# Kernel tuning notes

Hardware: AMD Instinct MI355X
Metric: run time of the kernel (lower is better)

Reference implementation:

```python
import jax, jax.numpy as jnp
import numpy as np
import math

D_MODEL = 512
N_HEADS = 8
HEAD_DIM = D_MODEL // N_HEADS          # 64
RANK = max(N_HEADS, int(D_MODEL * 0.25))  # 128
RPH = RANK // N_HEADS                  # 16
LN_EPS = 1e-12


def _rope_tables(L, head_dim, dtype=jnp.float32):
    half = head_dim // 2
    theta = 1.0 / (10000.0 ** (jnp.arange(half, dtype=dtype) / half))
    ang = jnp.arange(L, dtype=dtype)[:, None] * theta[None, :]   # [L, half]
    return jnp.cos(ang), jnp.sin(ang)


def _apply_rope(x, cos, sin):
    # x: [B, L, H, D]; pairs (even, odd) along D form complex numbers
    B, L, H, D = x.shape
    xr = x.reshape(B, L, H, D // 2, 2)
    xre, xim = xr[..., 0], xr[..., 1]
    c = cos[None, :, None, :]
    s = sin[None, :, None, :]
    out_re = xre * c - xim * s
    out_im = xre * s + xim * c
    return jnp.stack([out_re, out_im], axis=-1).reshape(B, L, H, D)


def _tpa(x, mask, Wq, Wk, Wv, U, V):
    # x: [B, L, C]; mask: [B, L] bool; Wq/Wk/Wv: [rank, C]; U: [H, hd, rph]; V: [H, rph, hd]
    B, L, C = x.shape
    H, hd, rph = U.shape
    q_low = (x @ Wq.T).reshape(B, L, H, rph)
    k_low = (x @ Wk.T).reshape(B, L, H, rph)
    v_low = (x @ Wv.T).reshape(B, L, H, rph)
    q = jnp.einsum('hdr,blhr->blhd', U, q_low)
    k = jnp.einsum('hdr,blhr->blhd', U, k_low)
    cos, sin = _rope_tables(L, hd, x.dtype)
    q = _apply_rope(q, cos, sin)
    k = _apply_rope(k, cos, sin)
    attn = jnp.einsum('blhd,bmhd->bhlm', q, k) / math.sqrt(hd)
    attn = jnp.where(mask[:, None, None, :], attn, -jnp.inf)
    attn = jax.nn.softmax(attn, axis=-1)
    out = jnp.einsum('bhlm,bmhr->blhr', attn, v_low)
    out = jnp.einsum('blhr,hrd->blhd', out, V)
    return out.reshape(B, L, C)


def _layer_norm(x, g, b):
    m = jnp.mean(x, axis=-1, keepdims=True)
    v = jnp.mean(jnp.square(x - m), axis=-1, keepdims=True)
    return (x - m) / jnp.sqrt(v + LN_EPS) * g + b


def setup_inputs() -> dict:
    key = jax.random.key(0)
    ks = jax.random.split(key, 24)
    B, T, L, C = 4, 64, 256, D_MODEL

    def lin(k, shp, fan):
        return jax.random.normal(k, shp, jnp.float32) * (1.0 / math.sqrt(fan))

    inp = {
        'x': jax.random.normal(ks[0], (B, T, L, C), jnp.float32),
        'mask': jnp.ones((B, T, L), dtype=bool),
        'pe': jax.random.normal(ks[1], (L, C), jnp.float32),
        # time TPA params
        't_Wq': lin(ks[2], (RANK, C), C), 't_Wk': lin(ks[3], (RANK, C), C), 't_Wv': lin(ks[4], (RANK, C), C),
        't_U': lin(ks[5], (N_HEADS, HEAD_DIM, RPH), HEAD_DIM + RPH),
        't_V': lin(ks[6], (N_HEADS, RPH, HEAD_DIM), HEAD_DIM + RPH),
        # aa TPA params
        'a_Wq': lin(ks[7], (RANK, C), C), 'a_Wk': lin(ks[8], (RANK, C), C), 'a_Wv': lin(ks[9], (RANK, C), C),
        'a_U': lin(ks[10], (N_HEADS, HEAD_DIM, RPH), HEAD_DIM + RPH),
        'a_V': lin(ks[11], (N_HEADS, RPH, HEAD_DIM), HEAD_DIM + RPH),
        # layer norms
        'ln1_g': jnp.ones((C,)), 'ln1_b': jnp.zeros((C,)),
        'ln2_g': jnp.ones((C,)), 'ln2_b': jnp.zeros((C,)),
        'ln3_g': jnp.ones((C,)), 'ln3_b': jnp.zeros((C,)),
        # proj + gates
        'proj_W': lin(ks[12], (C, C), C), 'proj_b': jnp.zeros((C,)),
        'gt_W': lin(ks[13], (C, 2 * C), 2 * C), 'gt_b': jnp.zeros((C,)),
        'ga_W': lin(ks[14], (C, 2 * C), 2 * C), 'ga_b': jnp.zeros((C,)),
    }
    return inp


def reference(x, mask, pe,
              t_Wq, t_Wk, t_Wv, t_U, t_V,
              a_Wq, a_Wk, a_Wv, a_U, a_V,
              ln1_g, ln1_b, ln2_g, ln2_b, ln3_g, ln3_b,
              proj_W, proj_b, gt_W, gt_b, ga_W, ga_b):
    B, T, L, C = x.shape
    residual_time = x
    xn = _layer_norm(x, ln1_g, ln1_b)
    # temporal attention over T, batched over (B*L)
    x_time = jnp.transpose(xn, (0, 2, 1, 3)).reshape(B * L, T, C)
    m_time = jnp.transpose(mask, (0, 2, 1)).reshape(B * L, T)
    x_time = _tpa(x_time, m_time, t_Wq, t_Wk, t_Wv, t_U, t_V)
    x_time = jnp.transpose(x_time.reshape(B, L, T, C), (0, 2, 1, 3))
    gate = jax.nn.sigmoid(jnp.concatenate([residual_time, x_time], axis=-1) @ gt_W.T + gt_b)
    x_time = gate * residual_time + (1.0 - gate) * x_time

    residual_aa = x_time
    xn2 = _layer_norm(x_time, ln2_g, ln2_b)
    # spatial (amino-acid) attention over L, batched over (B*T)
    x_aa = xn2.reshape(B * T, L, C)
    m_aa = mask.reshape(B * T, L)
    x_aa = _tpa(x_aa, m_aa, a_Wq, a_Wk, a_Wv, a_U, a_V)
    x_aa = x_aa.reshape(B, T, L, C)
    gate = jax.nn.sigmoid(jnp.concatenate([residual_aa, x_aa], axis=-1) @ ga_W.T + ga_b)
    x_aa = gate * residual_aa + (1.0 - gate) * x_aa

    residual_proj = x_aa
    x_aa = _layer_norm(x_aa, ln3_g, ln3_b) @ proj_W.T + proj_b  # dropout is identity in eval
    return x_aa + residual_proj
```

## Files before the change

kernel.cpp:

```cpp
#include <hip/hip_runtime.h>

typedef __attribute__((ext_vector_type(8))) short short8;
typedef __attribute__((ext_vector_type(4))) short short4v;
typedef __attribute__((ext_vector_type(4))) float f32x4;
typedef unsigned short ushort_t;
typedef unsigned int uint_t;

#define B_ 4
#define T_ 64
#define L_ 256
#define C_ 512
#define H_ 8
#define NTOK 65536

__device__ __forceinline__ ushort_t f2bf(float f) {
    uint_t u = __float_as_uint(f);
    u += 0x7FFFu + ((u >> 16) & 1u);
    return (ushort_t)(u >> 16);
}
__device__ __forceinline__ float bf2f(ushort_t u) {
    return __uint_as_float((uint_t)u << 16);
}
__device__ __forceinline__ uint_t pk2(float a, float b) {
    return (uint_t)f2bf(a) | ((uint_t)f2bf(b) << 16);
}
__device__ __forceinline__ void gload16(const ushort_t* __restrict__ g, ushort_t* l) {
    __builtin_amdgcn_global_load_lds(
        (const __attribute__((address_space(1))) void*)g,
        (__attribute__((address_space(3))) void*)l,
        16, 0, 0);
}

__global__ void rope_tables(float* __restrict__ cosT, float* __restrict__ sinT) {
    int idx = blockIdx.x * 256 + threadIdx.x;
    if (idx >= 256 * 32) return;
    int pos = idx >> 5, i = idx & 31;
    float theta = powf(10000.f, -(float)i * (1.f / 32.f));
    float ang = (float)pos * theta;
    float sv, cv;
    sincosf(ang, &sv, &cv);
    cosT[idx] = cv;
    sinT[idx] = sv;
}

__global__ void packw(const float* __restrict__ src, ushort_t* __restrict__ dst, int n) {
    const int i = (blockIdx.x * 256 + threadIdx.x) * 4;
    if (i < n) {
        float4 v = *(const float4*)(src + i);
        *(uint2*)(dst + i) = make_uint2(pk2(v.x, v.y), pk2(v.z, v.w));
    }
}

template<bool RAW>
__global__ void lnpack_f(const float* __restrict__ xin, const float* __restrict__ lng,
                         const float* __restrict__ lnbias, ushort_t* __restrict__ outb,
                         ushort_t* __restrict__ rawb) {
    const int lane = threadIdx.x & 63;
    const int w = threadIdx.x >> 6;
    const size_t tok = (size_t)blockIdx.x * 4 + w;
    const float* row = xin + tok * 512 + lane * 8;
    float4 a = *(const float4*)row;
    float4 b = *(const float4*)(row + 4);
    if (RAW) {
        uint4 rp = make_uint4(pk2(a.x, a.y), pk2(a.z, a.w), pk2(b.x, b.y), pk2(b.z, b.w));
        *(uint4*)(rawb + tok * 512 + lane * 8) = rp;
    }
    float s = a.x + a.y + a.z + a.w + b.x + b.y + b.z + b.w;
    float q = a.x*a.x + a.y*a.y + a.z*a.z + a.w*a.w + b.x*b.x + b.y*b.y + b.z*b.z + b.w*b.w;
    #pragma unroll
    for (int off = 32; off >= 1; off >>= 1) {
        s += __shfl_xor(s, off);
        q += __shfl_xor(q, off);
    }
    const float m = s * (1.f / 512.f);
    const float v = q * (1.f / 512.f) - m * m;
    const float rs = 1.f / sqrtf(v + 1e-12f);
    float4 gv0 = *(const float4*)(lng + lane * 8);
    float4 gv1 = *(const float4*)(lng + lane * 8 + 4);
    float4 bv0 = *(const float4*)(lnbias + lane * 8);
    float4 bv1 = *(const float4*)(lnbias + lane * 8 + 4);
    float o0 = (a.x - m) * rs * gv0.x + bv0.x;
    float o1 = (a.y - m) * rs * gv0.y + bv0.y;
    float o2 = (a.z - m) * rs * gv0.z + bv0.z;
    float o3 = (a.w - m) * rs * gv0.w + bv0.w;
    float o4 = (b.x - m) * rs * gv1.x + bv1.x;
    float o5 = (b.y - m) * rs * gv1.y + bv1.y;
    float o6 = (b.z - m) * rs * gv1.z + bv1.z;
    float o7 = (b.w - m) * rs * gv1.w + bv1.w;
    uint4 pk = make_uint4(pk2(o0, o1), pk2(o2, o3), pk2(o4, o5), pk2(o6, o7));
    *(uint4*)(outb + tok * 512 + lane * 8) = pk;
}

__global__ void lnpack_h(const ushort_t* __restrict__ xin, const float* __restrict__ lng,
                         const float* __restrict__ lnbias, ushort_t* __restrict__ outb) {
    const int lane = threadIdx.x & 63;
    const int w = threadIdx.x >> 6;
    const size_t tok = (size_t)blockIdx.x * 4 + w;
    const short8* rp = (const short8*)(xin + tok * 512 + lane * 8);
    const short8 r = rp[0];
    float x[8];
    #pragma unroll
    for (int jv = 0; jv < 8; ++jv) x[jv] = bf2f((ushort_t)r[jv]);
    float s = 0.f, q = 0.f;
    #pragma unroll
    for (int jv = 0; jv < 8; ++jv) { s += x[jv]; q += x[jv] * x[jv]; }
    #pragma unroll
    for (int off = 32; off >= 1; off >>= 1) {
        s += __shfl_xor(s, off);
        q += __shfl_xor(q, off);
    }
    const float m = s * (1.f / 512.f);
    const float v = q * (1.f / 512.f) - m * m;
    const float rs = 1.f / sqrtf(v + 1e-12f);
    float4 gv0 = *(const float4*)(lng + lane * 8);
    float4 gv1 = *(const float4*)(lng + lane * 8 + 4);
    float4 bv0 = *(const float4*)(lnbias + lane * 8);
    float4 bv1 = *(const float4*)(lnbias + lane * 8 + 4);
    float o[8];
    o[0] = (x[0] - m) * rs * gv0.x + bv0.x;
    o[1] = (x[1] - m) * rs * gv0.y + bv0.y;
    o[2] = (x[2] - m) * rs * gv0.z + bv0.z;
    o[3] = (x[3] - m) * rs * gv0.w + bv0.w;
    o[4] = (x[4] - m) * rs * gv1.x + bv1.x;
    o[5] = (x[5] - m) * rs * gv1.y + bv1.y;
    o[6] = (x[6] - m) * rs * gv1.z + bv1.z;
    o[7] = (x[7] - m) * rs * gv1.w + bv1.w;
    uint4 pk = make_uint4(pk2(o[0], o[1]), pk2(o[2], o[3]), pk2(o[4], o[5]), pk2(o[6], o[7]));
    *(uint4*)(outb + tok * 512 + lane * 8) = pk;
}

__global__ void fold_w(const float* __restrict__ Wq, const float* __restrict__ Wk,
                       const float* __restrict__ Wv, const float* __restrict__ U,
                       const float* __restrict__ V, ushort_t* __restrict__ Weff) {
    const int o = blockIdx.x;
    const int proj = o >> 9, orow = o & 511;
    const int h = orow >> 6, d = orow & 63;
    const float* W = (proj == 0) ? Wq : (proj == 1) ? Wk : Wv;
    float coef[16];
    #pragma unroll
    for (int r = 0; r < 16; ++r)
        coef[r] = (proj < 2) ? U[h * 1024 + d * 16 + r] : V[h * 1024 + r * 64 + d];
    const float scale = (proj == 0) ? 0.125f : 1.f;
    for (int c = threadIdx.x; c < 512; c += 256) {
        float acc = 0.f;
        #pragma unroll
        for (int r = 0; r < 16; ++r) acc += coef[r] * W[(h * 16 + r) * 512 + c];
        Weff[(long)o * 512 + c] = f2bf(acc * scale);
    }
}

template<bool TIME>
__launch_bounds__(512)
__global__ void gemm_qkv3(const ushort_t* __restrict__ Ab, const ushort_t* __restrict__ Wb,
                          const float* __restrict__ cosT, const float* __restrict__ sinT,
                          ushort_t* __restrict__ Cout) {
    __shared__ __align__(16) char arena[24576];
    ushort_t* AsL = (ushort_t*)arena;
    ushort_t* BsL = AsL + 4096;
    ushort_t (*Ebuf)[72] = (ushort_t (*)[72])arena;

    const int id = blockIdx.x;
    const int xcd = id & 7;
    const int j = id >> 3;
    const int mBase = (xcd * 64 + j / 6) * 128;
    const int nBase = (j % 6) * 256;

    const int tid = threadIdx.x;
    const int lane = tid & 63;
    const int w8 = tid >> 6;

    f32x4 zero = {0.f, 0.f, 0.f, 0.f};
    f32x4 acc[4][4];
    #pragma unroll
    for (int a = 0; a < 4; ++a)
        #pragma unroll
        for (int b = 0; b < 4; ++b) acc[a][b] = zero;

    const int wr = w8 >> 2, wc = w8 & 3;
    const int l15 = lane & 15;
    const int g = lane >> 4;
    const int arw = wr * 64 + l15;
    const int brw = wc * 64 + l15;

    const int qa = (w8 << 6) + lane;
    const int ra = qa >> 2;
    const int ca = (qa & 3) ^ ((ra >> 1) & 3);
    const long gsrcA = (long)(mBase + ra) * 512 + ca * 8;
    ushort_t* ldsA = AsL + (w8 << 9);

    int rb[2], cb[2];
    #pragma unroll
    for (int i = 0; i < 2; ++i) {
        const int qb = (w8 << 7) + (i << 6) + lane;
        rb[i] = qb >> 2;
        cb[i] = (qb & 3) ^ ((rb[i] >> 1) & 3);
    }

    for (int kt = 0; kt < 512; kt += 32) {
        __syncthreads();
        gload16(Ab + gsrcA + kt, ldsA);
        #pragma unroll
        for (int i = 0; i < 2; ++i)
            gload16(Wb + (long)(nBase + rb[i]) * 512 + kt + cb[i] * 8,
                    BsL + (w8 << 10) + (i << 9));
        __syncthreads();

        short8 af[4], bf[4];
        #pragma unroll
        for (int mi = 0; mi < 4; ++mi) {
            const int R = arw + mi * 16;
            af[mi] = *(const short8*)(AsL + R * 32 + ((g ^ ((R >> 1) & 3)) * 8));
        }
        #pragma unroll
        for (int ni = 0; ni < 4; ++ni) {
            const int R = brw + ni * 16;
            bf[ni] = *(const short8*)(BsL + R * 32 + ((g ^ ((R >> 1) & 3)) * 8));
        }
        #pragma unroll
        for (int mi = 0; mi < 4; ++mi)
            #pragma unroll
            for (int ni = 0; ni < 4; ++ni)
                acc[mi][ni] = __builtin_amdgcn_mfma_f32_16x16x32_bf16(af[mi], bf[ni], acc[mi][ni], 0, 0, 0);
    }

    #pragma unroll 1
    for (int s = 0; s < 4; ++s) {
        __syncthreads();
        if (wc == s) {
            #pragma unroll
            for (int mi = 0; mi < 4; ++mi)
                #pragma unroll
                for (int ni = 0; ni < 4; ++ni)
                    #pragma unroll
                    for (int jj = 0; jj < 4; ++jj)
                        Ebuf[wr * 64 + mi * 16 + g * 4 + jj][ni * 16 + l15] =
                            f2bf(acc[mi][ni][jj]);
        }
        __syncthreads();
        #pragma unroll
        for (int it = 0; it < 2; ++it) {
            const int u = tid + it * 512;
            const int row = u >> 3, c8 = u & 7;
            short8 v8 = *(const short8*)&Ebuf[row][c8 * 8];
            const long grow = mBase + row;
            const int gcol = nBase + s * 64 + c8 * 8;
            ushort_t* dst = Cout + grow * 1536 + gcol;
            if (gcol < 1024) {
                const int pos = TIME ? ((int)(grow >> 8) & 63) : ((int)grow & 255);
                const float* cT = cosT + pos * 32 + c8 * 4;
                const float* sT = sinT + pos * 32 + c8 * 4;
                uint_t pkv[4];
                #pragma unroll
                for (int p = 0; p < 4; ++p) {
                    const float cc = cT[p], ss = sT[p];
                    const float re = bf2f((ushort_t)v8[2 * p]);
                    const float im = bf2f((ushort_t)v8[2 * p + 1]);
                    pkv[p] = pk2(re * cc - im * ss, re * ss + im * cc);
                }
                *(uint4*)dst = make_uint4(pkv[0], pkv[1], pkv[2], pkv[3]);
            } else {
                *(short8*)dst = v8;
            }
        }
    }
}

template<int EPI>
__launch_bounds__(512)
__global__ void gemm256(const ushort_t* __restrict__ A1b, const ushort_t* __restrict__ A2b,
                        const ushort_t* __restrict__ Bwb, void* __restrict__ Cout_,
                        const float* __restrict__ bias, const ushort_t* __restrict__ R1b,
                        const ushort_t* __restrict__ R2b) {
    constexpr int K = (EPI == 1) ? 1024 : 512;
    __shared__ __align__(16) char arena[24576];
    ushort_t* AsL = (ushort_t*)arena;
    ushort_t* BsL = AsL + 4096;

    const int id = blockIdx.x;
    const int xcd = id & 7;
    const int j = id >> 3;
    const int mBase = (xcd * 64 + (j >> 1)) * 128;
    const int nBase = (j & 1) * 256;

    const int tid = threadIdx.x;
    const int lane = tid & 63;
    const int w8 = tid >> 6;

    f32x4 zero = {0.f, 0.f, 0.f, 0.f};
    f32x4 acc[4][4];
    #pragma unroll
    for (int a = 0; a < 4; ++a)
        #pragma unroll
        for (int b = 0; b < 4; ++b) acc[a][b] = zero;

    const int wr = w8 >> 2, wc = w8 & 3;
    const int l15 = lane & 15;
    const int g = lane >> 4;
    const int arw = wr * 64 + l15;
    const int brw = wc * 64 + l15;

    const int qa = (w8 << 6) + lane;
    const int ra = qa >> 2;
    const int ca = (qa & 3) ^ ((ra >> 1) & 3);
    ushort_t* ldsA = AsL + (w8 << 9);

    int rb[2], cb[2];
    #pragma unroll
    for (int i = 0; i < 2; ++i) {
        const int qb = (w8 << 7) + (i << 6) + lane;
        rb[i] = qb >> 2;
        cb[i] = (qb & 3) ^ ((rb[i] >> 1) & 3);
    }

    for (int kt = 0; kt < K; kt += 32) {
        const ushort_t* Abase = (EPI == 1 && kt >= 512) ? A2b : A1b;
        const int kcol = (EPI == 1 && kt >= 512) ? kt - 512 : kt;

        __syncthreads();
        gload16(Abase + (long)(mBase + ra) * 512 + kcol + ca * 8, ldsA);
        #pragma unroll
        for (int i = 0; i < 2; ++i)
            gload16(Bwb + (long)(nBase + rb[i]) * K + kt + cb[i] * 8,
                    BsL + (w8 << 10) + (i << 9));
        __syncthreads();

        short8 af[4], bf[4];
        #pragma unroll
        for (int mi = 0; mi < 4; ++mi) {
            const int R = arw + mi * 16;
            af[mi] = *(const short8*)(AsL + R * 32 + ((g ^ ((R >> 1) & 3)) * 8));
        }
        #pragma unroll
        for (int ni = 0; ni < 4; ++ni) {
            const int R = brw + ni * 16;
            bf[ni] = *(const short8*)(BsL + R * 32 + ((g ^ ((R >> 1) & 3)) * 8));
        }
        #pragma unroll
        for (int mi = 0; mi < 4; ++mi)
            #pragma unroll
            for (int ni = 0; ni < 4; ++ni)
                acc[mi][ni] = __builtin_amdgcn_mfma_f32_16x16x32_bf16(af[mi], bf[ni], acc[mi][ni], 0, 0, 0);
    }

    #pragma unroll
    for (int mi = 0; mi < 4; ++mi) {
        #pragma unroll
        for (int ni = 0; ni < 4; ++ni) {
            #pragma unroll
            for (int jj = 0; jj < 4; ++jj) {
                const long row = mBase + wr * 64 + mi * 16 + ((lane >> 4) << 2) + jj;
                const long col = nBase + wc * 64 + ni * 16 + l15;
                const long idx = row * 512 + col;
                const float v = acc[mi][ni][jj];
                if (EPI == 1) {
                    const float z = v + bias[col];
                    const float gg = 1.f / (1.f + __expf(-z));
                    const float o = gg * bf2f(R1b[idx]) + (1.f - gg) * bf2f(R2b[idx]);
                    ((ushort_t*)Cout_)[idx] = f2bf(o);
                } else {
                    ((float*)Cout_)[idx] = v + bias[col] + bf2f(R1b[idx]);
                }
            }
        }
    }
}

template<int SEQ, bool TIME>
__launch_bounds__(256)
__global__ void attn3(const ushort_t* __restrict__ qkve, ushort_t* __restrict__ xattn) {
    constexpr int NCH = SEQ / 64;
    constexpr int NQT = SEQ / 64;
    constexpr int NPART = 256 / SEQ;
    constexpr int DCH = 8 / NPART;

    __shared__ short Klds[SEQ][64];
    __shared__ short VTs[64][SEQ];
    __shared__ short Pw[4][16][40];

    const int bx = blockIdx.x;
    const int h = bx & 7;
    const int grp = bx >> 3;
    int tokBase, tokStride;
    if (TIME) {
        const int l = grp & (L_ - 1);
        const int b = grp >> 8;
        tokBase = b * T_ * L_ + l;
        tokStride = L_;
    } else {
        tokBase = grp * L_;
        tokStride = 1;
    }
    const int tid = threadIdx.x;
    const int lane = tid & 63;
    const int w = tid >> 6;

    {
        const int key = tid & (SEQ - 1);
        const int part = tid / SEQ;
        const long tok = tokBase + (long)key * tokStride;
        const ushort_t* kb = qkve + tok * 1536 + 512 + h * 64;
        const ushort_t* vb = qkve + tok * 1536 + 1024 + h * 64;
        #pragma unroll
        for (int c = 0; c < DCH; ++c) {
            const int chunk = part * DCH + c;
            const short8 kv = *(const short8*)(kb + chunk * 8);
            *(short8*)&Klds[key][(chunk ^ (key & 7)) * 8] = kv;
            const short8 vv = *(const short8*)(vb + chunk * 8);
            #pragma unroll
            for (int jx = 0; jx < 8; ++jx) {
                const int d = chunk * 8 + jx;
                VTs[d][(((key >> 3) ^ (d & 7)) * 8) + (key & 7)] = vv[jx];
            }
        }
    }
    __syncthreads();

    const int l15 = lane & 15;
    const int g = lane >> 4;

    #pragma unroll 1
    for (int qt = 0; qt < NQT; ++qt) {
        const int qbase = qt * 64 + w * 16;
        const long qtok = tokBase + (long)(qbase + l15) * tokStride;

        const ushort_t* qb = qkve + qtok * 1536 + h * 64;
        const short8 Qf0 = *(const short8*)(qb + g * 8);
        const short8 Qf1 = *(const short8*)(qb + 32 + g * 8);

        f32x4 O[4];
        #pragma unroll
        for (int nj = 0; nj < 4; ++nj) { f32x4 z = {0.f,0.f,0.f,0.f}; O[nj] = z; }
        float psum = 0.f;

        #pragma unroll 1
        for (int kb2 = 0; kb2 < NCH; ++kb2) {
            f32x4 S[4];
            #pragma unroll
            for (int f4 = 0; f4 < 4; ++f4) {
                const int row = kb2 * 64 + f4 * 16 + l15;
                const short8 a0 = *(const short8*)&Klds[row][((0 + g) ^ (l15 & 7)) * 8];
                const short8 a1 = *(const short8*)&Klds[row][((4 + g) ^ (l15 & 7)) * 8];
                f32x4 z = {0.f, 0.f, 0.f, 0.f};
                z = __builtin_amdgcn_mfma_f32_16x16x32_bf16(a0, Qf0, z, 0, 0, 0);
                S[f4] = __builtin_amdgcn_mfma_f32_16x16x32_bf16(a1, Qf1, z, 0, 0, 0);
            }
            #pragma unroll
            for (int f4 = 0; f4 < 4; ++f4)
                #pragma unroll
                for (int jj = 0; jj < 4; ++jj) {
                    const float p = __expf(fminf(S[f4][jj], 30.f));
                    S[f4][jj] = p;
                    psum += p;
                }

            #pragma unroll
            for (int sl = 0; sl < 2; ++sl) {
                #pragma unroll
                for (int h2 = 0; h2 < 2; ++h2) {
                    const int f4 = 2 * sl + h2;
                    short4v pv;
                    pv[0] = (short)f2bf(S[f4][0]);
                    pv[1] = (short)f2bf(S[f4][1]);
                    pv[2] = (short)f2bf(S[f4][2]);
                    pv[3] = (short)f2bf(S[f4][3]);
                    *(short4v*)&Pw[w][l15][h2 * 16 + 4 * g] = pv;
                }
                const short8 pa = *(const short8*)&Pw[w][l15][8 * g];
                const int sg = kb2 * 2 + sl;
                #pragma unroll
                for (int nj = 0; nj < 4; ++nj) {
                    const int row = nj * 16 + l15;
                    const short8 bv = *(const short8*)&VTs[row][((4 * sg + g) ^ (l15 & 7)) * 8];
                    O[nj] = __builtin_amdgcn_mfma_f32_16x16x32_bf16(pa, bv, O[nj], 0, 0, 0);
                }
            }
        }

        psum += __shfl_xor(psum, 16);
        psum += __shfl_xor(psum, 32);
        const float inv = 1.f / psum;
        #pragma unroll
        for (int jj = 0; jj < 4; ++jj) {
            const float invq = __shfl(inv, 4 * g + jj);
            const long row = tokBase + (long)(qbase + 4 * g + jj) * tokStride;
            ushort_t* op = xattn + row * 512 + h * 64 + l15;
            #pragma unroll
            for (int nj = 0; nj < 4; ++nj)
                op[nj * 16] = f2bf(O[nj][jj] * invq);
        }
    }
}

extern "C" void kernel_launch(void* const* d_in, const int* in_sizes, int n_in,
                              void* d_out, int out_size, void* d_ws, size_t ws_size,
                              hipStream_t stream) {
    const float* x      = (const float*)d_in[0];
    const float* t_Wq   = (const float*)d_in[3];
    const float* t_Wk   = (const float*)d_in[4];
    const float* t_Wv   = (const float*)d_in[5];
    const float* t_U    = (const float*)d_in[6];
    const float* t_V    = (const float*)d_in[7];
    const float* a_Wq   = (const float*)d_in[8];
    const float* a_Wk   = (const float*)d_in[9];
    const float* a_Wv   = (const float*)d_in[10];
    const float* a_U    = (const float*)d_in[11];
    const float* a_V    = (const float*)d_in[12];
    const float* ln1_g  = (const float*)d_in[13];
    const float* ln1_b  = (const float*)d_in[14];
    const float* ln2_g  = (const float*)d_in[15];
    const float* ln2_b  = (const float*)d_in[16];
    const float* ln3_g  = (const float*)d_in[17];
    const float* ln3_b  = (const float*)d_in[18];
    const float* proj_W = (const float*)d_in[19];
    const float* proj_b = (const float*)d_in[20];
    const float* gt_W   = (const float*)d_in[21];
    const float* gt_b   = (const float*)d_in[22];
    const float* ga_W   = (const float*)d_in[23];
    const float* ga_b   = (const float*)d_in[24];
    float* out = (float*)d_out;

    const size_t NC = (size_t)NTOK * 512;
    ushort_t* xb   = (ushort_t*)d_ws;
    ushort_t* lnb  = xb + NC;
    ushort_t* resA = lnb + NC;
    ushort_t* qkve = resA + NC;
    ushort_t* resB = qkve;
    ushort_t* Weff = qkve + (size_t)NTOK * 1536;
    ushort_t* gtWb = Weff + 1536 * 512;
    ushort_t* gaWb = gtWb + 512 * 1024;
    ushort_t* prWb = gaWb + 512 * 1024;
    float* cosT = (float*)(prWb + 512 * 512);
    float* sinT = cosT + 8192;
    ushort_t* xattb = lnb;

    rope_tables<<<32, 256, 0, stream>>>(cosT, sinT);
    packw<<<512, 256, 0, stream>>>(gt_W, gtWb, 512 * 1024);
    packw<<<512, 256, 0, stream>>>(ga_W, gaWb, 512 * 1024);
    packw<<<256, 256, 0, stream>>>(proj_W, prWb, 512 * 512);

    fold_w<<<1536, 256, 0, stream>>>(t_Wq, t_Wk, t_Wv, t_U, t_V, Weff);
    lnpack_f<true><<<NTOK / 4, 256, 0, stream>>>(x, ln1_g, ln1_b, lnb, xb);
    gemm_qkv3<true><<<3072, 512, 0, stream>>>(lnb, Weff, cosT, sinT, qkve);
    attn3<64, true><<<B_ * L_ * H_, 256, 0, stream>>>(qkve, xattb);
    gemm256<1><<<1024, 512, 0, stream>>>(xb, xattb, gtWb, resA, gt_b, xb, xattb);

    fold_w<<<1536, 256, 0, stream>>>(a_Wq, a_Wk, a_Wv, a_U, a_V, Weff);
    lnpack_h<<<NTOK / 4, 256, 0, stream>>>(resA, ln2_g, ln2_b, lnb);
    gemm_qkv3<false><<<3072, 512, 0, stream>>>(lnb, Weff, cosT, sinT, qkve);
    attn3<256, false><<<B_ * T_ * H_, 256, 0, stream>>>(qkve, xattb);
    gemm256<1><<<1024, 512, 0, stream>>>(resA, xattb, gaWb, resB, ga_b, resA, xattb);

    lnpack_h<<<NTOK / 4, 256, 0, stream>>>(resB, ln3_g, ln3_b, lnb);
    gemm256<2><<<1024, 512, 0, stream>>>(lnb, nullptr, prWb, out, proj_b, resB, nullptr);
}
```

Measured before the change: 813.2 us.

## Double-buffer LDS tiles in QKV and 256-wide GEMM kernels

Both the QKV-projection GEMM and the generic 256-column GEMM now use two LDS tile buffers. The next K-slice is loaded into the idle buffer while MFMAs run on the current one. This removes one of the two barriers per K-step and lets global-to-LDS traffic overlap with compute. The cost is twice the LDS per block (48KB), which may reduce how many blocks fit on a CU. Correctness depends on the end-of-iteration barrier also waiting for the outstanding async loads.

```diff
diff --git a/kernel.cpp b/kernel.cpp
--- a/kernel.cpp
+++ b/kernel.cpp
@@ -154,9 +154,7 @@
 __global__ void gemm_qkv3(const ushort_t* __restrict__ Ab, const ushort_t* __restrict__ Wb,
                           const float* __restrict__ cosT, const float* __restrict__ sinT,
                           ushort_t* __restrict__ Cout) {
-    __shared__ __align__(16) char arena[24576];
-    ushort_t* AsL = (ushort_t*)arena;
-    ushort_t* BsL = AsL + 4096;
+    __shared__ __align__(16) char arena[49152];
     ushort_t (*Ebuf)[72] = (ushort_t (*)[72])arena;
 
     const int id = blockIdx.x;
@@ -185,25 +183,37 @@
     const int qa = (w8 << 6) + lane;
     const int ra = qa >> 2;
     const int ca = (qa & 3) ^ ((ra >> 1) & 3);
-    const long gsrcA = (long)(mBase + ra) * 512 + ca * 8;
-    ushort_t* ldsA = AsL + (w8 << 9);
-
-    int rb[2], cb[2];
+    const ushort_t* srcA = Ab + (long)(mBase + ra) * 512 + ca * 8;
+
+    const ushort_t* srcB[2];
     #pragma unroll
     for (int i = 0; i < 2; ++i) {
         const int qb = (w8 << 7) + (i << 6) + lane;
-        rb[i] = qb >> 2;
-        cb[i] = (qb & 3) ^ ((rb[i] >> 1) & 3);
-    }
-
+        const int rbv = qb >> 2;
+        const int cbv = (qb & 3) ^ ((rbv >> 1) & 3);
+        srcB[i] = Wb + (long)(nBase + rbv) * 512 + cbv * 8;
+    }
+
+    {
+        ushort_t* base = (ushort_t*)arena;
+        gload16(srcA, base + (w8 << 9));
+        gload16(srcB[0], base + 4096 + (w8 << 10));
+        gload16(srcB[1], base + 4096 + (w8 << 10) + 512);
+    }
+    asm volatile("s_waitcnt vmcnt(0)" ::: "memory");
+    __syncthreads();
+
+    #pragma unroll 1
     for (int kt = 0; kt < 512; kt += 32) {
-        __syncthreads();
-        gload16(Ab + gsrcA + kt, ldsA);
-        #pragma unroll
-        for (int i = 0; i < 2; ++i)
-            gload16(Wb + (long)(nBase + rb[i]) * 512 + kt + cb[i] * 8,
-                    BsL + (w8 << 10) + (i << 9));
-        __syncthreads();
+        const int cur = (kt >> 5) & 1;
+        if (kt + 32 < 512) {
+            ushort_t* nb = (ushort_t*)(arena + (cur ^ 1) * 24576);
+            gload16(srcA + kt + 32, nb + (w8 << 9));
+            gload16(srcB[0] + kt + 32, nb + 4096 + (w8 << 10));
+            gload16(srcB[1] + kt + 32, nb + 4096 + (w8 << 10) + 512);
+        }
+        ushort_t* AsL = (ushort_t*)(arena + cur * 24576);
+        ushort_t* BsL = AsL + 4096;
 
         short8 af[4], bf[4];
         #pragma unroll
@@ -221,6 +231,8 @@
             #pragma unroll
             for (int ni = 0; ni < 4; ++ni)
                 acc[mi][ni] = __builtin_amdgcn_mfma_f32_16x16x32_bf16(af[mi], bf[ni], acc[mi][ni], 0, 0, 0);
+
+        __syncthreads();
     }
 
     #pragma unroll 1
@@ -272,9 +284,7 @@
                         const float* __restrict__ bias, const ushort_t* __restrict__ R1b,
                         const ushort_t* __restrict__ R2b) {
     constexpr int K = (EPI == 1) ? 1024 : 512;
-    __shared__ __align__(16) char arena[24576];
-    ushort_t* AsL = (ushort_t*)arena;
-    ushort_t* BsL = AsL + 4096;
+    __shared__ __align__(16) char arena[49152];
 
     const int id = blockIdx.x;
     const int xcd = id & 7;
@@ -302,27 +312,40 @@
     const int qa = (w8 << 6) + lane;
     const int ra = qa >> 2;
     const int ca = (qa & 3) ^ ((ra >> 1) & 3);
-    ushort_t* ldsA = AsL + (w8 << 9);
-
-    int rb[2], cb[2];
+    const long offA = (long)(mBase + ra) * 512 + ca * 8;
+
+    const ushort_t* srcB[2];
     #pragma unroll
     for (int i = 0; i < 2; ++i) {
         const int qb = (w8 << 7) + (i << 6) + lane;
-        rb[i] = qb >> 2;
-        cb[i] = (qb & 3) ^ ((rb[i] >> 1) & 3);
-    }
-
+        const int rbv = qb >> 2;
+        const int cbv = (qb & 3) ^ ((rbv >> 1) & 3);
+        srcB[i] = Bwb + (long)(nBase + rbv) * K + cbv * 8;
+    }
+
+    {
+        ushort_t* base = (ushort_t*)arena;
+        gload16(A1b + offA, base + (w8 << 9));
+        gload16(srcB[0], base + 4096 + (w8 << 10));
+        gload16(srcB[1], base + 4096 + (w8 << 10) + 512);
+    }
+    asm volatile("s_waitcnt vmcnt(0)" ::: "memory");
+    __syncthreads();
+
+    #pragma unroll 1
     for (int kt = 0; kt < K; kt += 32) {
-        const ushort_t* Abase = (EPI == 1 && kt >= 512) ? A2b : A1b;
-        const int kcol = (EPI == 1 && kt >= 512) ? kt - 512 : kt;
-
-        __syncthreads();
-        gload16(Abase + (long)(mBase + ra) * 512 + kcol + ca * 8, ldsA);
-        #pragma unroll
-        for (int i = 0; i < 2; ++i)
-            gload16(Bwb + (long)(nBase + rb[i]) * K + kt + cb[i] * 8,
-                    BsL + (w8 << 10) + (i << 9));
-        __syncthreads();
+        const int cur = (kt >> 5) & 1;
+        if (kt + 32 < K) {
+            const int kn = kt + 32;
+            const ushort_t* an = (EPI == 1 && kn >= 512) ? (A2b + offA + (kn - 512))
+                                                         : (A1b + offA + kn);
+            ushort_t* nb = (ushort_t*)(arena + (cur ^ 1) * 24576);
+            gload16(an, nb + (w8 << 9));
+            gload16(srcB[0] + kn, nb + 4096 + (w8 << 10));
+            gload16(srcB[1] + kn, nb + 4096 + (w8 << 10) + 512);
+        }
+        ushort_t* AsL = (ushort_t*)(arena + cur * 24576);
+        ushort_t* BsL = AsL + 4096;
 
         short8 af[4], bf[4];
         #pragma unroll
@@ -340,6 +363,8 @@
             #pragma unroll
             for (int ni = 0; ni < 4; ++ni)
                 acc[mi][ni] = __builtin_amdgcn_mfma_f32_16x16x32_bf16(af[mi], bf[ni], acc[mi][ni], 0, 0, 0);
+
+        __syncthreads();
     }
 
     #pragma unroll
```

After: 803.2 us. About the same (-1.2%).
